# Performance work log

Hardware: AMD Instinct MI355X
Metric: run time of the kernel (lower is better)

## Reference

```python
import jax, jax.numpy as jnp
from jax import lax
import numpy as np
import math

B, T, D_IN, H, L, NDIR = 32, 512, 1024, 512, 2, 2


def setup_inputs() -> dict:
    key = jax.random.key(0)
    ks = jax.random.split(key, 5)
    std = 1.0 / math.sqrt(H)  # torch init: uniform(-std, std)
    u = lambda k, shape: jax.random.uniform(k, shape, jnp.float32, -std, std)
    return {
        "x": jax.random.normal(ks[0], (B, T, D_IN), jnp.float32),
        "Wx": u(ks[1], (L, NDIR, D_IN, 4 * H)),   # x2h weight (in, 4H)
        "bx": u(ks[2], (L, NDIR, 4 * H)),
        "Wh": u(ks[3], (L, NDIR, H, 4 * H)),      # h2h weight (H, 4H)
        "bh": u(ks[4], (L, NDIR, 4 * H)),
    }


def _lstm_dir(xs, Wx, bx, Wh, bh):
    """xs: [T,B,Din]; returns hs [T,B,H], (hT, cT)."""
    # precompute input projection for all timesteps (one big GEMM)
    gx = jnp.einsum('tbd,dg->tbg', xs, Wx) + bx + bh  # [T,B,4H]
    h0 = jnp.zeros((xs.shape[1], Wh.shape[0]), xs.dtype)

    def step(carry, gx_t):
        h, c = carry
        gates = gx_t + h @ Wh  # [B,4H]
        i, f, g, o = jnp.split(gates, 4, axis=-1)  # torch chunk order: i,f,g,o
        i = jax.nn.sigmoid(i)
        f = jax.nn.sigmoid(f)
        g = jnp.tanh(g)
        o = jax.nn.sigmoid(o)
        c = c * f + i * g
        h = o * jnp.tanh(c)
        return (h, c), h

    (hT, cT), hs = lax.scan(step, (h0, h0), gx)
    return hs, hT, cT


def reference(x, Wx, bx, Wh, bh):
    # x: [B,T,D_IN] (batch_first) -> time-major
    inputs = jnp.swapaxes(x, 0, 1)  # [T,B,D]
    h_list, c_list = [], []
    for layer in range(L):
        outs_dirs = []
        for d in range(NDIR):
            xs = inputs if d == 0 else inputs[::-1]
            hs, hT, cT = _lstm_dir(xs, Wx[layer, d], bx[layer, d], Wh[layer, d], bh[layer, d])
            outs_dirs.append(hs if d == 0 else hs[::-1])
            h_list.append(hT)
            c_list.append(cT)
        inputs = jnp.concatenate(outs_dirs, axis=-1)  # [T,B,2H] (dropout=0 / eval)
    output = jnp.swapaxes(inputs, 0, 1)  # [B,T,2H]
    h_n = jnp.stack(h_list)  # [L*NDIR, B, H]
    c_n = jnp.stack(c_list)
    return output, h_n, c_n
```

## Files before the change

kernel.cpp:

```cpp
#include <hip/hip_runtime.h>
#include <hip/hip_bf16.h>

#define DEV __device__ __forceinline__

typedef __bf16 bf16;
typedef __bf16 bf16x8 __attribute__((ext_vector_type(8)));
typedef float f32x4 __attribute__((ext_vector_type(4)));
typedef int i32x4 __attribute__((ext_vector_type(4)));
typedef unsigned int u32;

#define BB 32
#define TT 512
#define DIN 1024
#define HH 512
#define G4 2048
#define MM (TT*BB)

DEV float sigmf(float x){ return 1.0f/(1.0f + __expf(-x)); }
DEV float tanhfast(float x){ return 1.0f - 2.0f/(__expf(2.0f*x)+1.0f); }

DEV void gload16(const void* g, void* l){
  __builtin_amdgcn_global_load_lds((const __attribute__((address_space(1))) void*)g,
                                   (__attribute__((address_space(3))) void*)l, 16, 0, 0);
}

DEV i32x4 cload16(const void* p){
  i32x4 v;
  asm volatile("global_load_dwordx4 %0, %1, off sc0 sc1"
               : "=&v"(v) : "v"(p) : "memory");
  return v;
}
DEV void cstore16(void* p, i32x4 v){
  asm volatile("global_store_dwordx4 %0, %1, off sc0 sc1"
               :: "v"(p), "v"(v) : "memory");
}
DEV void cstore4(void* p, u32 v){
  asm volatile("global_store_dword %0, %1, off sc0 sc1"
               :: "v"(p), "v"(v) : "memory");
}
DEV u32 cload4(const void* p){
  u32 v;
  asm volatile("global_load_dword %0, %1, off sc0 sc1\n\ts_waitcnt vmcnt(0)"
               : "=&v"(v) : "v"(p) : "memory");
  return v;
}
DEV void waitvm0(){ asm volatile("s_waitcnt vmcnt(0)" ::: "memory"); }

__global__ void k_dbg(float* out, float v){ out[0] = v; }

__global__ void k_prep_bias(const float* __restrict__ bx, const float* __restrict__ bh,
                            float* __restrict__ bsum, u32* __restrict__ ctr){
  int gid = blockIdx.x*256 + threadIdx.x;
  if (gid < 4*G4) bsum[gid] = bx[gid] + bh[gid];
  if (gid < 128) cstore4(ctr + gid, 0u);
}

__global__ void k_xswz(const float* __restrict__ x, bf16* __restrict__ xs){
  int gid = blockIdx.x*256 + threadIdx.x;
  int r = gid >> 7, kc = gid & 127;
  int b = r & 31, t = r >> 5;
  const float* px = x + ((size_t)b*TT + t)*DIN + kc*8;
  float4 v0 = *(const float4*)px;
  float4 v1 = *(const float4*)(px+4);
  bf16x8 o;
  o[0]=(bf16)v0.x; o[1]=(bf16)v0.y; o[2]=(bf16)v0.z; o[3]=(bf16)v0.w;
  o[4]=(bf16)v1.x; o[5]=(bf16)v1.y; o[6]=(bf16)v1.z; o[7]=(bf16)v1.w;
  *(bf16x8*)(xs + (size_t)r*DIN + ((kc ^ (r&7))<<3)) = o;
}

__global__ void k_twx(const float* __restrict__ Wx, bf16* __restrict__ Wxt){
  int ld = blockIdx.z;
  int k0 = blockIdx.x*64, n0 = blockIdx.y*64;
  const float* in = Wx + (size_t)ld*DIN*G4;
  bf16* outp = Wxt + (size_t)ld*G4*DIN;
  __shared__ float tile[64][68];
  int tid = threadIdx.x;
  #pragma unroll
  for (int rr=0; rr<4; rr++){
    int row = rr*16 + (tid>>4); int c4 = (tid&15)*4;
    float4 v = *(const float4*)(in + (size_t)(k0+row)*G4 + n0 + c4);
    *(float4*)&tile[row][c4] = v;
  }
  __syncthreads();
  #pragma unroll
  for (int uu=0; uu<2; uu++){
    int u = uu*256 + tid;
    int nn = u>>3, ck = u&7;
    bf16x8 o;
    #pragma unroll
    for (int j=0;j<8;j++) o[j] = (bf16)tile[ck*8+j][nn];
    int ncol = n0 + nn;
    int kcg = (k0>>3) + ck;
    *(bf16x8*)(outp + (size_t)ncol*DIN + ((size_t)(kcg ^ (ncol&7))<<3)) = o;
  }
}

__global__ void k_twh(const float* __restrict__ Wh, bf16* __restrict__ Whb){
  int ld = blockIdx.z;
  int k0 = blockIdx.x*64, n0 = blockIdx.y*64;
  const float* in = Wh + (size_t)ld*HH*G4;
  bf16* outp = Whb + (size_t)ld*G4*HH;
  __shared__ float tile[64][68];
  int tid = threadIdx.x;
  #pragma unroll
  for (int rr=0; rr<4; rr++){
    int row = rr*16 + (tid>>4); int c4 = (tid&15)*4;
    float4 v = *(const float4*)(in + (size_t)(k0+row)*G4 + n0 + c4);
    *(float4*)&tile[row][c4] = v;
  }
  __syncthreads();
  #pragma unroll
  for (int uu=0; uu<2; uu++){
    int u = uu*256 + tid;
    int nn = u>>3, ck = u&7;
    bf16x8 o;
    #pragma unroll
    for (int j=0;j<8;j++) o[j] = (bf16)tile[ck*8+j][nn];
    int n = n0 + nn;
    int q = n >> 9, rem = n & 511;
    int s = rem >> 4, wq = (rem >> 2) & 3, hcv = rem & 3;
    int cc = s*64 + wq*16 + q*4 + hcv;
    *(bf16x8*)(outp + (size_t)cc*HH + k0 + ck*8) = o;
  }
}

template<typename GXT>
__launch_bounds__(256, 1)
__global__ void k_gemm(const bf16* __restrict__ A, const bf16* __restrict__ Bw,
                       const float* __restrict__ bias, GXT* __restrict__ out){
  int d = blockIdx.z;
  const bf16* Bp = Bw + (size_t)d*G4*DIN;
  const float* bp = bias + d*G4;
  GXT* op = out + (size_t)d*MM*G4;
  int n0 = blockIdx.x*128, r0 = blockIdx.y*128;
  int tid = threadIdx.x, lane = tid&63, w = tid>>6;
  __shared__ __align__(16) bf16 ldsA[128*64];
  __shared__ __align__(16) bf16 ldsB[128*64];
  f32x4 acc[4][4];
  #pragma unroll
  for (int i=0;i<4;i++)
    #pragma unroll
    for (int j=0;j<4;j++) acc[i][j] = (f32x4){0.f,0.f,0.f,0.f};
  int wm = w>>1, wn = w&1;
  for (int kt=0; kt<16; kt++){
    __syncthreads();
    #pragma unroll
    for (int p=0;p<4;p++){
      int seg = p*4 + w;
      int row = seg*8 + (lane>>3);
      int cch = lane&7;
      gload16(A  + (size_t)(r0+row)*DIN + kt*64 + cch*8, ldsA + seg*512);
      gload16(Bp + (size_t)(n0+row)*DIN + kt*64 + cch*8, ldsB + seg*512);
    }
    __syncthreads();
    #pragma unroll
    for (int ks=0; ks<2; ks++){
      bf16x8 af[4], bf_[4];
      #pragma unroll
      for (int at=0; at<4; at++){
        int row = wm*64 + at*16 + (lane&15);
        int ch = (ks*4 + (lane>>4)) ^ (row&7);
        af[at] = *(const bf16x8*)(ldsA + row*64 + ch*8);
      }
      #pragma unroll
      for (int bt=0; bt<4; bt++){
        int col = wn*64 + bt*16 + (lane&15);
        int ch = (ks*4 + (lane>>4)) ^ (col&7);
        bf_[bt] = *(const bf16x8*)(ldsB + col*64 + ch*8);
      }
      #pragma unroll
      for (int at=0; at<4; at++)
        #pragma unroll
        for (int bt=0; bt<4; bt++)
          acc[at][bt] = __builtin_amdgcn_mfma_f32_16x16x32_bf16(af[at], bf_[bt], acc[at][bt], 0,0,0);
    }
  }
  float bv[4];
  #pragma unroll
  for (int bt=0;bt<4;bt++) bv[bt] = bp[n0 + wn*64 + bt*16 + (lane&15)];
  #pragma unroll
  for (int at=0; at<4; at++)
    #pragma unroll
    for (int bt=0; bt<4; bt++)
      #pragma unroll
      for (int rg=0; rg<4; rg++){
        int row = r0 + wm*64 + at*16 + (lane>>4)*4 + rg;
        int col = n0 + wn*64 + bt*16 + (lane&15);
        op[(size_t)row*G4 + col] = (GXT)(acc[at][bt][rg] + bv[bt]);
      }
}

template<typename GXT>
__launch_bounds__(256, 1)
__global__ void k_rec(const bf16* __restrict__ Whb, const GXT* __restrict__ gx,
                      bf16* __restrict__ hbuf, u32* __restrict__ ctr,
                      bf16* __restrict__ out0, float* __restrict__ dout,
                      float* __restrict__ hn, float* __restrict__ cn, int layer, int dir0){
  int tid = threadIdx.x, lane = tid&63, w = tid>>6;
  int dl = blockIdx.x >> 5, s = blockIdx.x & 31;
  int d = dir0 + dl;
  __shared__ __align__(16) bf16 hA[32*512];
  __shared__ __align__(16) bf16 hOut[32*16];
  const bf16* Wp = Whb + ((size_t)d*G4 + s*64 + w*16 + (lane&15))*HH;
  bf16x8 bfr[16];
  #pragma unroll
  for (int kk=0; kk<16; kk++) bfr[kk] = *(const bf16x8*)(Wp + kk*32 + (lane>>4)*8);
  float cst[2][4] = {{0,0,0,0},{0,0,0,0}};
  const GXT* gxD = gx + (size_t)dl*MM*G4;
  u32* cbase = ctr + dl*32;
  u32* myctr = cbase + s;
  int q = (lane>>2)&3, hc = lane&3;
  int colg = q*HH + s*16 + w*4 + hc;
  int m0 = lane&15;
  bool hi = (q >= 2), odd = (q & 1);

  for (int t=0; t<TT; t++){
    int tt = d ? (TT-1-t) : t;
    float gxv[2][4];
    {
      const GXT* gp = gxD + (size_t)tt*BB*G4 + colg;
      #pragma unroll
      for (int mt=0; mt<2; mt++)
        #pragma unroll
        for (int rg=0; rg<4; rg++)
          gxv[mt][rg] = (float)gp[(size_t)(mt*16 + (lane>>4)*4 + rg)*G4];
    }
    f32x4 acc0 = {0.f,0.f,0.f,0.f}, acc1 = {0.f,0.f,0.f,0.f};
    if (t > 0){
      if (w == 1){
        u32 me = lane & 31;
        while (true){
          u32 v = cload4(cbase + me);
          if (__ballot(v >= (u32)t) == ~0ull) break;
          __builtin_amdgcn_s_sleep(2);
        }
      }
      __syncthreads();
      const bf16* hsrc = hbuf + ((size_t)d*2 + ((t-1)&1))*BB*HH;
      i32x4 hreg[8];
      #pragma unroll
      for (int i=0;i<8;i++){
        int chunk = i*256 + tid;
        int b = chunk>>6, j = chunk&63;
        hreg[i] = cload16(hsrc + b*HH + j*8);
      }
      waitvm0();
      __builtin_amdgcn_sched_barrier(0);
      #pragma unroll
      for (int i=0;i<8;i++){
        int chunk = i*256 + tid;
        int b = chunk>>6, j = chunk&63;
        *(i32x4*)(hA + b*HH + ((j ^ (b&7))<<3)) = hreg[i];
      }
      __syncthreads();
      #pragma unroll
      for (int kk=0; kk<16; kk++){
        int ch = (kk*4 + (lane>>4)) ^ (m0&7);
        bf16x8 a0 = *(const bf16x8*)(hA + m0*HH + ch*8);
        bf16x8 a1 = *(const bf16x8*)(hA + (m0+16)*HH + ch*8);
        acc0 = __builtin_amdgcn_mfma_f32_16x16x32_bf16(a0, bfr[kk], acc0, 0,0,0);
        acc1 = __builtin_amdgcn_mfma_f32_16x16x32_bf16(a1, bfr[kk], acc1, 0,0,0);
      }
    }
    #pragma unroll
    for (int mt=0; mt<2; mt++){
      #pragma unroll
      for (int rg=0; rg<4; rg++){
        float gpre = (mt ? acc1[rg] : acc0[rg]) + gxv[mt][rg];
        float x4  = __shfl_xor(gpre, 4);
        float x8  = __shfl_xor(gpre, 8);
        float x12 = __shfl_xor(gpre, 12);
        float a04 = odd ? x4 : gpre,  b04 = odd ? gpre : x4;
        float a812 = odd ? x12 : x8,  b812 = odd ? x8 : x12;
        float ig = hi ? a812 : a04;
        float fg = hi ? b812 : b04;
        float gg = hi ? a04 : a812;
        float og = hi ? b04 : b812;
        float iv = sigmf(ig), fv = sigmf(fg), gv = tanhfast(gg), ov = sigmf(og);
        float c = cst[mt][rg]*fv + iv*gv;
        cst[mt][rg] = c;
        float hvv = ov * tanhfast(c);
        if (q == 0){
          int b = mt*16 + (lane>>4)*4 + rg;
          hOut[b*16 + w*4 + hc] = (bf16)hvv;
          if (layer == 1)
            __builtin_nontemporal_store(hvv,
              dout + ((size_t)(b*TT + tt))*(2*HH) + d*HH + s*16 + w*4 + hc);
          if (t == TT-1)
            hn[((size_t)((layer*2+d)*BB + b))*HH + s*16 + w*4 + hc] = hvv;
        }
      }
    }
    if (t == TT-1 && q == 0){
      #pragma unroll
      for (int mt=0; mt<2; mt++)
        #pragma unroll
        for (int rg=0; rg<4; rg++){
          int b = mt*16 + (lane>>4)*4 + rg;
          cn[((size_t)((layer*2+d)*BB + b))*HH + s*16 + w*4 + hc] = cst[mt][rg];
        }
    }
    __syncthreads();
    if (w == 0){
      int b = lane>>1, half = lane&1;
      i32x4 v = *(const i32x4*)(hOut + b*16 + half*8);
      cstore16(hbuf + ((size_t)d*2 + (t&1))*BB*HH + b*HH + s*16 + half*8, v);
      waitvm0();
      if (lane == 0) cstore4(myctr, (u32)(t+1));
      if (layer == 0){
        int r = tt*BB + b;
        int chunk = (d*64 + s*2 + half) ^ (r&7);
        __builtin_nontemporal_store(*(const bf16x8*)&v,
                                    (bf16x8*)(out0 + (size_t)r*DIN + chunk*8));
      }
    }
  }
}

extern "C" void kernel_launch(void* const* d_in, const int* in_sizes, int n_in,
                              void* d_out, int out_size, void* d_ws, size_t ws_size,
                              hipStream_t stream){
  const float* x  = (const float*)d_in[0];
  const float* Wx = (const float*)d_in[1];
  const float* bx = (const float*)d_in[2];
  const float* Wh = (const float*)d_in[3];
  const float* bh = (const float*)d_in[4];
  float* outp = (float*)d_out;
  char* ws = (char*)d_ws;

  const size_t szWxt  = (size_t)4*G4*DIN*2;
  const size_t szWhb  = (size_t)4*G4*HH*2;
  const size_t szBsum = (size_t)4*G4*4;
  const size_t szXO   = (size_t)MM*DIN*2;
  const size_t szHbuf = (size_t)2*2*BB*HH*2;
  const size_t szCtr  = 512;

  int mode = -1;
  size_t oWxt=0,oWhb=0,oBsum=0,oXO=0,oOut0=0,oHbuf=0,oCtr=0,oGx=0;
  for (int m=0; m<3 && mode<0; m++){
    size_t off = 0;
    auto take = [&](size_t b)->size_t{ size_t r = off; off = (off + b + 255) & ~(size_t)255; return r; };
    oWxt = take(szWxt); oWhb = take(szWhb); oBsum = take(szBsum);
    oXO  = take(szXO);
    oOut0 = (m==2) ? take(szXO) : oXO;
    oHbuf = take(szHbuf); oCtr = take(szCtr);
    size_t gxb = (m==0) ? (size_t)2*MM*G4*4 : (m==1) ? (size_t)2*MM*G4*2 : (size_t)MM*G4*2;
    oGx = take(gxb);
    if (off <= ws_size) mode = m;
  }
  if (mode < 0){
    k_dbg<<<1, 1, 0, stream>>>(outp, (float)((double)ws_size / 1048576.0));
    return;
  }

  bf16* Wxt  = (bf16*)(ws + oWxt);
  bf16* Whb  = (bf16*)(ws + oWhb);
  float* bsum= (float*)(ws + oBsum);
  bf16* xo   = (bf16*)(ws + oXO);
  bf16* out0 = (bf16*)(ws + oOut0);
  bf16* hbuf = (bf16*)(ws + oHbuf);
  u32*  ctr  = (u32*)(ws + oCtr);
  void* gxp  = (void*)(ws + oGx);

  float* hn = outp + (size_t)BB*TT*2*HH;
  float* cn = hn + (size_t)4*BB*HH;

  k_prep_bias<<<32, 256, 0, stream>>>(bx, bh, bsum, ctr);
  k_xswz<<<(MM*128)/256, 256, 0, stream>>>(x, xo);
  k_twx<<<dim3(16,32,4), 256, 0, stream>>>(Wx, Wxt);
  k_twh<<<dim3(8,32,4), 256, 0, stream>>>(Wh, Whb);

  if (mode == 0){
    float* gx = (float*)gxp;
    for (int layer=0; layer<2; layer++){
      k_gemm<float><<<dim3(16,128,2), 256, 0, stream>>>(xo, Wxt + (size_t)layer*2*G4*DIN,
                                                        bsum + layer*2*G4, gx);
      k_rec<float><<<64, 256, 0, stream>>>(Whb + (size_t)layer*2*G4*HH, gx, hbuf,
                                           ctr + layer*64, out0, outp, hn, cn, layer, 0);
    }
  } else if (mode == 1){
    bf16* gx = (bf16*)gxp;
    for (int layer=0; layer<2; layer++){
      k_gemm<bf16><<<dim3(16,128,2), 256, 0, stream>>>(xo, Wxt + (size_t)layer*2*G4*DIN,
                                                       bsum + layer*2*G4, gx);
      k_rec<bf16><<<64, 256, 0, stream>>>(Whb + (size_t)layer*2*G4*HH, gx, hbuf,
                                          ctr + layer*64, out0, outp, hn, cn, layer, 0);
    }
  } else {
    bf16* gx = (bf16*)gxp;
    for (int layer=0; layer<2; layer++){
      const bf16* A = layer ? out0 : xo;
      for (int dd=0; dd<2; dd++){
        k_gemm<bf16><<<dim3(16,128,1), 256, 0, stream>>>(A, Wxt + (size_t)(layer*2+dd)*G4*DIN,
                                                         bsum + (layer*2+dd)*G4, gx);
        k_rec<bf16><<<32, 256, 0, stream>>>(Whb + (size_t)layer*2*G4*HH, gx, hbuf,
                                            ctr + (layer*2+dd)*32, out0, outp, hn, cn, layer, dd);
      }
    }
  }
}
```

Before: 6.716 ms.

## Replace counter-based step barrier with tagged hidden-state packets in recurrence

New measurement: 5.624 ms. 1.19x faster.

```diff
diff --git a/kernel.cpp b/kernel.cpp
--- a/kernel.cpp
+++ b/kernel.cpp
@@ -8,6 +8,7 @@
 typedef float f32x4 __attribute__((ext_vector_type(4)));
 typedef int i32x4 __attribute__((ext_vector_type(4)));
 typedef unsigned int u32;
+typedef unsigned long long u64;
 
 #define BB 32
 #define TT 512
@@ -15,6 +16,7 @@
 #define HH 512
 #define G4 2048
 #define MM (TT*BB)
+#define TAGMAGIC 0x5A000000u
 
 DEV float sigmf(float x){ return 1.0f/(1.0f + __expf(-x)); }
 DEV float tanhfast(float x){ return 1.0f - 2.0f/(__expf(2.0f*x)+1.0f); }
@@ -34,25 +36,14 @@
   asm volatile("global_store_dwordx4 %0, %1, off sc0 sc1"
                :: "v"(p), "v"(v) : "memory");
 }
-DEV void cstore4(void* p, u32 v){
-  asm volatile("global_store_dword %0, %1, off sc0 sc1"
-               :: "v"(p), "v"(v) : "memory");
-}
-DEV u32 cload4(const void* p){
-  u32 v;
-  asm volatile("global_load_dword %0, %1, off sc0 sc1\n\ts_waitcnt vmcnt(0)"
-               : "=&v"(v) : "v"(p) : "memory");
-  return v;
-}
 DEV void waitvm0(){ asm volatile("s_waitcnt vmcnt(0)" ::: "memory"); }
 
 __global__ void k_dbg(float* out, float v){ out[0] = v; }
 
 __global__ void k_prep_bias(const float* __restrict__ bx, const float* __restrict__ bh,
-                            float* __restrict__ bsum, u32* __restrict__ ctr){
+                            float* __restrict__ bsum){
   int gid = blockIdx.x*256 + threadIdx.x;
   if (gid < 4*G4) bsum[gid] = bx[gid] + bh[gid];
-  if (gid < 128) cstore4(ctr + gid, 0u);
 }
 
 __global__ void k_xswz(const float* __restrict__ x, bf16* __restrict__ xs){
@@ -193,22 +184,21 @@
 template<typename GXT>
 __launch_bounds__(256, 1)
 __global__ void k_rec(const bf16* __restrict__ Whb, const GXT* __restrict__ gx,
-                      bf16* __restrict__ hbuf, u32* __restrict__ ctr,
+                      char* __restrict__ hbT,
                       bf16* __restrict__ out0, float* __restrict__ dout,
                       float* __restrict__ hn, float* __restrict__ cn, int layer, int dir0){
   int tid = threadIdx.x, lane = tid&63, w = tid>>6;
   int dl = blockIdx.x >> 5, s = blockIdx.x & 31;
   int d = dir0 + dl;
   __shared__ __align__(16) bf16 hA[32*512];
-  __shared__ __align__(16) bf16 hOut[32*16];
+  __shared__ __align__(8) unsigned short hP[4*128];
   const bf16* Wp = Whb + ((size_t)d*G4 + s*64 + w*16 + (lane&15))*HH;
   bf16x8 bfr[16];
   #pragma unroll
   for (int kk=0; kk<16; kk++) bfr[kk] = *(const bf16x8*)(Wp + kk*32 + (lane>>4)*8);
   float cst[2][4] = {{0,0,0,0},{0,0,0,0}};
   const GXT* gxD = gx + (size_t)dl*MM*G4;
-  u32* cbase = ctr + dl*32;
-  u32* myctr = cbase + s;
+  const u32 tagbase = TAGMAGIC + (u32)((layer*2 + d)*TT);
   int q = (lane>>2)&3, hc = lane&3;
   int colg = q*HH + s*16 + w*4 + hc;
   int m0 = lane&15;
@@ -216,41 +206,41 @@
 
   for (int t=0; t<TT; t++){
     int tt = d ? (TT-1-t) : t;
-    float gxv[2][4];
+    GXT gxr[2][4];
     {
       const GXT* gp = gxD + (size_t)tt*BB*G4 + colg;
       #pragma unroll
       for (int mt=0; mt<2; mt++)
         #pragma unroll
         for (int rg=0; rg<4; rg++)
-          gxv[mt][rg] = (float)gp[(size_t)(mt*16 + (lane>>4)*4 + rg)*G4];
+          gxr[mt][rg] = gp[(size_t)(mt*16 + (lane>>4)*4 + rg)*G4];
     }
     f32x4 acc0 = {0.f,0.f,0.f,0.f}, acc1 = {0.f,0.f,0.f,0.f};
     if (t > 0){
-      if (w == 1){
-        u32 me = lane & 31;
-        while (true){
-          u32 v = cload4(cbase + me);
-          if (__ballot(v >= (u32)t) == ~0ull) break;
-          __builtin_amdgcn_s_sleep(2);
-        }
-      }
-      __syncthreads();
-      const bf16* hsrc = hbuf + ((size_t)d*2 + ((t-1)&1))*BB*HH;
-      i32x4 hreg[8];
-      #pragma unroll
-      for (int i=0;i<8;i++){
-        int chunk = i*256 + tid;
-        int b = chunk>>6, j = chunk&63;
-        hreg[i] = cload16(hsrc + b*HH + j*8);
-      }
+      const char* sT = hbT + ((size_t)(dl*2 + ((t-1)&1)) << 16);
+      u32 want = tagbase + (u32)t;
+      i32x4 u[16];
+      #pragma unroll
+      for (int i=0;i<16;i++){ int g = i*256 + tid; u[i] = cload16(sT + ((size_t)g<<4)); }
       waitvm0();
       __builtin_amdgcn_sched_barrier(0);
-      #pragma unroll
-      for (int i=0;i<8;i++){
-        int chunk = i*256 + tid;
-        int b = chunk>>6, j = chunk&63;
-        *(i32x4*)(hA + b*HH + ((j ^ (b&7))<<3)) = hreg[i];
+      while (true){
+        bool bad = false;
+        #pragma unroll
+        for (int i=0;i<16;i++) bad |= ((u32)u[i].z != want);
+        if (!__any(bad)) break;
+        __builtin_amdgcn_s_sleep(1);
+        #pragma unroll
+        for (int i=0;i<16;i++) if ((u32)u[i].z != want){ int g = i*256 + tid; u[i] = cload16(sT + ((size_t)g<<4)); }
+        waitvm0();
+        __builtin_amdgcn_sched_barrier(0);
+      }
+      __syncthreads();
+      #pragma unroll
+      for (int i=0;i<16;i++){
+        int g = i*256 + tid; int b = g>>7, cu = g&127;
+        u64 dat = ((u64)(u32)u[i].y << 32) | (u32)u[i].x;
+        *(u64*)((char*)hA + b*1024 + ((((cu>>1) ^ (b&7)))<<4) + (cu&1)*8) = dat;
       }
       __syncthreads();
       #pragma unroll
@@ -266,7 +256,7 @@
     for (int mt=0; mt<2; mt++){
       #pragma unroll
       for (int rg=0; rg<4; rg++){
-        float gpre = (mt ? acc1[rg] : acc0[rg]) + gxv[mt][rg];
+        float gpre = (mt ? acc1[rg] : acc0[rg]) + (float)gxr[mt][rg];
         float x4  = __shfl_xor(gpre, 4);
         float x8  = __shfl_xor(gpre, 8);
         float x12 = __shfl_xor(gpre, 12);
@@ -282,7 +272,7 @@
         float hvv = ov * tanhfast(c);
         if (q == 0){
           int b = mt*16 + (lane>>4)*4 + rg;
-          hOut[b*16 + w*4 + hc] = (bf16)hvv;
+          hP[w*128 + b*4 + hc] = __builtin_bit_cast(unsigned short, (bf16)hvv);
           if (layer == 1)
             __builtin_nontemporal_store(hvv,
               dout + ((size_t)(b*TT + tt))*(2*HH) + d*HH + s*16 + w*4 + hc);
@@ -300,18 +290,21 @@
           cn[((size_t)((layer*2+d)*BB + b))*HH + s*16 + w*4 + hc] = cst[mt][rg];
         }
     }
-    __syncthreads();
-    if (w == 0){
-      int b = lane>>1, half = lane&1;
-      i32x4 v = *(const i32x4*)(hOut + b*16 + half*8);
-      cstore16(hbuf + ((size_t)d*2 + (t&1))*BB*HH + b*HH + s*16 + half*8, v);
-      waitvm0();
-      if (lane == 0) cstore4(myctr, (u32)(t+1));
+    if (lane < 32){
+      u64 d8 = *(const u64*)(hP + w*128 + lane*4);
+      if (t < TT-1){
+        char* dT = hbT + ((size_t)(dl*2 + (t&1)) << 16);
+        i32x4 unit;
+        unit.x = (int)(u32)(d8 & 0xffffffffu);
+        unit.y = (int)(u32)(d8 >> 32);
+        unit.z = (int)(tagbase + (u32)t + 1u);
+        unit.w = 0;
+        cstore16(dT + ((size_t)(lane*128 + s*4 + w) << 4), unit);
+      }
       if (layer == 0){
-        int r = tt*BB + b;
-        int chunk = (d*64 + s*2 + half) ^ (r&7);
-        __builtin_nontemporal_store(*(const bf16x8*)&v,
-                                    (bf16x8*)(out0 + (size_t)r*DIN + chunk*8));
+        int r = tt*BB + lane;
+        int c = d*64 + s*2 + (w>>1);
+        *(u64*)(out0 + (size_t)r*DIN + (size_t)(c ^ (r&7))*8 + (w&1)*4) = d8;
       }
     }
   }
@@ -332,18 +325,17 @@
   const size_t szWhb  = (size_t)4*G4*HH*2;
   const size_t szBsum = (size_t)4*G4*4;
   const size_t szXO   = (size_t)MM*DIN*2;
-  const size_t szHbuf = (size_t)2*2*BB*HH*2;
-  const size_t szCtr  = 512;
+  const size_t szHbT  = (size_t)2*2*4096*16;
 
   int mode = -1;
-  size_t oWxt=0,oWhb=0,oBsum=0,oXO=0,oOut0=0,oHbuf=0,oCtr=0,oGx=0;
+  size_t oWxt=0,oWhb=0,oBsum=0,oXO=0,oOut0=0,oHbT=0,oGx=0;
   for (int m=0; m<3 && mode<0; m++){
     size_t off = 0;
     auto take = [&](size_t b)->size_t{ size_t r = off; off = (off + b + 255) & ~(size_t)255; return r; };
     oWxt = take(szWxt); oWhb = take(szWhb); oBsum = take(szBsum);
     oXO  = take(szXO);
     oOut0 = (m==2) ? take(szXO) : oXO;
-    oHbuf = take(szHbuf); oCtr = take(szCtr);
+    oHbT = take(szHbT);
     size_t gxb = (m==0) ? (size_t)2*MM*G4*4 : (m==1) ? (size_t)2*MM*G4*2 : (size_t)MM*G4*2;
     oGx = take(gxb);
     if (off <= ws_size) mode = m;
@@ -358,14 +350,14 @@
   float* bsum= (float*)(ws + oBsum);
   bf16* xo   = (bf16*)(ws + oXO);
   bf16* out0 = (bf16*)(ws + oOut0);
-  bf16* hbuf = (bf16*)(ws + oHbuf);
-  u32*  ctr  = (u32*)(ws + oCtr);
+  char* hbT  = ws + oHbT;
   void* gxp  = (void*)(ws + oGx);
 
   float* hn = outp + (size_t)BB*TT*2*HH;
   float* cn = hn + (size_t)4*BB*HH;
 
-  k_prep_bias<<<32, 256, 0, stream>>>(bx, bh, bsum, ctr);
+  hipMemsetAsync(hbT, 0, szHbT, stream);
+  k_prep_bias<<<32, 256, 0, stream>>>(bx, bh, bsum);
   k_xswz<<<(MM*128)/256, 256, 0, stream>>>(x, xo);
   k_twx<<<dim3(16,32,4), 256, 0, stream>>>(Wx, Wxt);
   k_twh<<<dim3(8,32,4), 256, 0, stream>>>(Wh, Whb);
@@ -375,16 +367,16 @@
     for (int layer=0; layer<2; layer++){
       k_gemm<float><<<dim3(16,128,2), 256, 0, stream>>>(xo, Wxt + (size_t)layer*2*G4*DIN,
                                                         bsum + layer*2*G4, gx);
-      k_rec<float><<<64, 256, 0, stream>>>(Whb + (size_t)layer*2*G4*HH, gx, hbuf,
-                                           ctr + layer*64, out0, outp, hn, cn, layer, 0);
+      k_rec<float><<<64, 256, 0, stream>>>(Whb + (size_t)layer*2*G4*HH, gx, hbT,
+                                           out0, outp, hn, cn, layer, 0);
     }
   } else if (mode == 1){
     bf16* gx = (bf16*)gxp;
     for (int layer=0; layer<2; layer++){
       k_gemm<bf16><<<dim3(16,128,2), 256, 0, stream>>>(xo, Wxt + (size_t)layer*2*G4*DIN,
                                                        bsum + layer*2*G4, gx);
-      k_rec<bf16><<<64, 256, 0, stream>>>(Whb + (size_t)layer*2*G4*HH, gx, hbuf,
-                                          ctr + layer*64, out0, outp, hn, cn, layer, 0);
+      k_rec<bf16><<<64, 256, 0, stream>>>(Whb + (size_t)layer*2*G4*HH, gx, hbT,
+                                          out0, outp, hn, cn, layer, 0);
     }
   } else {
     bf16* gx = (bf16*)gxp;
@@ -393,9 +385,9 @@
       for (int dd=0; dd<2; dd++){
         k_gemm<bf16><<<dim3(16,128,1), 256, 0, stream>>>(A, Wxt + (size_t)(layer*2+dd)*G4*DIN,
                                                          bsum + (layer*2+dd)*G4, gx);
-        k_rec<bf16><<<32, 256, 0, stream>>>(Whb + (size_t)layer*2*G4*HH, gx, hbuf,
-                                            ctr + (layer*2+dd)*32, out0, outp, hn, cn, layer, dd);
-      }
-    }
-  }
-}
+        k_rec<bf16><<<32, 256, 0, stream>>>(Whb + (size_t)layer*2*G4*HH, gx, hbT,
+                                            out0, outp, hn, cn, layer, dd);
+      }
+    }
+  }
+}
```
